# Kernel optimization log

Measured on AMD Instinct MI355X. Metric: run time of the kernel, lower is better.

## Reference

```python
import jax, jax.numpy as jnp
import numpy as np

TWO_PI = 2.0 * np.pi
EPS = 1e-08


def setup_inputs() -> dict:
    key = jax.random.key(0)
    k1, k2, k3 = jax.random.split(key, 3)
    N, D = 1048576, 64
    samples = jax.random.normal(k1, (N, D), dtype=jnp.float32)
    Phi = jax.random.uniform(k2, (1,), dtype=jnp.float32)
    # mu init in torch: 2*rand - 0.5
    mu = 2.0 * jax.random.uniform(k3, (D,), dtype=jnp.float32) - 0.5
    Sigma = jnp.eye(D, dtype=jnp.float32)
    return {"samples": samples, "Phi": Phi, "mu": mu, "Sigma": Sigma}


def reference(samples, Phi, mu, Sigma):
    # Batched Mahalanobis quadratic form replacing the per-sample Python loop.
    inv_sigma = jnp.linalg.pinv(Sigma)                      # [D, D]
    det_sigma = jnp.linalg.det(Sigma)                       # scalar
    diff = samples - mu                                     # [N, D]
    # q_n = diff_n^T inv_sigma diff_n
    q = jnp.einsum('nd,de,ne->n', diff, inv_sigma, diff)    # [N]
    dens = Phi[0] * jnp.exp(-0.5 * q) / jnp.sqrt(TWO_PI * det_sigma)
    return -jnp.log(dens + EPS)                             # with_log=True path
```

## Files before the change

### kernel.cpp

```cpp
#include <hip/hip_runtime.h>


typedef __attribute__((ext_vector_type(8))) short s8bf;
typedef __attribute__((ext_vector_type(4))) float v4f;

#define TWO_PI_F 6.2831853071795864769f

__device__ __forceinline__ float bf2f(ushort u) {
    union { float f; unsigned int i; } v; v.i = ((unsigned int)u) << 16; return v.f;
}
__device__ __forceinline__ ushort f2bf(float f) {
    unsigned int x = __float_as_uint(f);
    return (ushort)((x + 0x7fffu + ((x >> 16) & 1u)) >> 16);
}
__device__ __forceinline__ s8bf pack8(float4 a, float4 b) {
    s8bf r;
    r[0] = (short)f2bf(a.x); r[1] = (short)f2bf(a.y);
    r[2] = (short)f2bf(a.z); r[3] = (short)f2bf(a.w);
    r[4] = (short)f2bf(b.x); r[5] = (short)f2bf(b.y);
    r[6] = (short)f2bf(b.z); r[7] = (short)f2bf(b.w);
    return r;
}

__global__ __launch_bounds__(256) void prep_kernel(const void* __restrict__ Sigma,
                                                   const void* __restrict__ Phi,
                                                   const void* __restrict__ mu,
                                                   void* __restrict__ ws) {
    __shared__ __align__(16) float colbuf[64];
    __shared__ __align__(16) float rowbuf[64];
    __shared__ __align__(16) float sA[64 * 65];
    __shared__ float smu[64];
    const int t = threadIdx.x;
    const int j = t & 63, w = t >> 6;
    const unsigned int wd0 = *(const unsigned int*)Sigma;
    const bool isf32 = (wd0 == 0x3F800000u);

    float ar[16];
    if (isf32) {
        const float* S = (const float*)Sigma;
#pragma unroll
        for (int ii = 0; ii < 16; ++ii) ar[ii] = S[(16 * w + ii) * 64 + j];
    } else {
        const ushort* S = (const ushort*)Sigma;
#pragma unroll
        for (int ii = 0; ii < 16; ++ii) ar[ii] = bf2f(S[(16 * w + ii) * 64 + j]);
    }
    if (t < 64) smu[t] = isf32 ? ((const float*)mu)[t] : bf2f(((const ushort*)mu)[t]);

    float det = 1.0f;
    for (int k = 0; k < 64; ++k) {
        if (j == k) {
#pragma unroll
            for (int ii = 0; ii < 16; ++ii) colbuf[16 * w + ii] = ar[ii];
        }
        if (w == (k >> 4)) {
            float val = ar[0];
#pragma unroll
            for (int ii = 1; ii < 16; ++ii) val = (ii == (k & 15)) ? ar[ii] : val;
            rowbuf[j] = val;
        }
        __syncthreads();
        const float piv = rowbuf[k];
        const float ip = 1.0f / piv;
        const float rk = rowbuf[j] * ip;
        det *= piv;
        const bool jk = (j == k);
#pragma unroll
        for (int ii = 0; ii < 16; ++ii) {
            float f = colbuf[16 * w + ii];
            float nv = fmaf(-f, rk, ar[ii]);
            nv = jk ? (-f * ip) : nv;
            if (16 * w + ii == k) nv = jk ? ip : rk;
            ar[ii] = nv;
        }
        __syncthreads();
    }

    ushort* wb = (ushort*)ws;
#pragma unroll
    for (int ii = 0; ii < 16; ++ii) wb[(16 * w + ii) * 64 + j] = f2bf(ar[ii]);
#pragma unroll
    for (int ii = 0; ii < 16; ++ii) sA[(16 * w + ii) * 65 + j] = ar[ii];
    __syncthreads();

    float* wf = (float*)((char*)ws + 8192);
    if (t < 64) {
        float dot = 0.0f;
#pragma unroll
        for (int jj = 0; jj < 64; ++jj) dot = fmaf(sA[t * 65 + jj], smu[jj], dot);
        wf[t] = 2.0f * dot;
        float pc = smu[t] * dot;
#pragma unroll
        for (int off = 1; off < 64; off <<= 1) pc += __shfl_xor(pc, off, 64);
        if (t == 0) {
            float ph = isf32 ? ((const float*)Phi)[0] : bf2f(((const ushort*)Phi)[0]);
            wf[64] = pc;
            wf[65] = ph / sqrtf(TWO_PI_F * det);
            wf[66] = isf32 ? 1.0f : 0.0f;
        }
    }
}

__global__ __launch_bounds__(256) void gmm_kernel(const void* __restrict__ Xv,
                                                  const void* __restrict__ ws,
                                                  void* __restrict__ outv,
                                                  int ntiles) {
    __shared__ __align__(16) ushort sB[64 * 72];
    __shared__ __align__(16) ushort sX[64 * 64];
    const int t = threadIdx.x;
    const int w = t >> 6, l = t & 63, n = l & 15, q = l >> 4;

    const ushort* wb = (const ushort*)ws;
#pragma unroll
    for (int p0 = 0; p0 < 2; ++p0) {
        int idx = p0 * 2048 + t * 8;
        int r = idx >> 6, c = idx & 63;
        *(uint4*)(&sB[r * 72 + c]) = *(const uint4*)(wb + idx);
    }
    const float* wf = (const float*)((const char*)ws + 8192);
    float vneg[4];
#pragma unroll
    for (int c = 0; c < 4; ++c) vneg[c] = -wf[c * 16 + n];
    const float c0 = wf[64], sc = wf[65];
    const bool isf32 = (wf[66] != 0.0f);
    __syncthreads();

    s8bf bfr[2][4];
#pragma unroll
    for (int s = 0; s < 2; ++s)
#pragma unroll
        for (int c = 0; c < 4; ++c)
            bfr[s][c] = *(const s8bf*)(&sB[(c * 16 + n) * 72 + s * 32 + q * 8]);

    const int sr = t >> 2, h = t & 3;
    const int c0i = 2 * h, c1i = 2 * h + 1;
    ushort* dst0 = sX + sr * 64 + ((c0i ^ (sr & 7)) * 8);
    ushort* dst1 = sX + sr * 64 + ((c1i ^ (sr & 7)) * 8);

    for (int tile = blockIdx.x; tile < ntiles; tile += gridDim.x) {
        s8bf ch0, ch1;
        if (isf32) {
            const float* src = (const float*)Xv + (size_t)tile * 4096 + sr * 64 + h * 16;
            float4 f0 = ((const float4*)src)[0];
            float4 f1 = ((const float4*)src)[1];
            float4 f2 = ((const float4*)src)[2];
            float4 f3 = ((const float4*)src)[3];
            ch0 = pack8(f0, f1);
            ch1 = pack8(f2, f3);
        } else {
            const ushort* src = (const ushort*)Xv + (size_t)tile * 4096 + sr * 64 + h * 16;
            ch0 = ((const s8bf*)src)[0];
            ch1 = ((const s8bf*)src)[1];
        }
        __syncthreads();
        *(s8bf*)dst0 = ch0;
        *(s8bf*)dst1 = ch1;
        __syncthreads();

        v4f acc[4];
#pragma unroll
        for (int c = 0; c < 4; ++c) acc[c] = (v4f){vneg[c], vneg[c], vneg[c], vneg[c]};

#pragma unroll
        for (int s = 0; s < 2; ++s) {
            int chunk = (4 * s + q) ^ (n & 7);
            s8bf af = *(const s8bf*)(sX + (w * 16 + n) * 64 + chunk * 8);
#pragma unroll
            for (int c = 0; c < 4; ++c)
                acc[c] = __builtin_amdgcn_mfma_f32_16x16x32_bf16(af, bfr[s][c], acc[c], 0, 0, 0);
        }

        float p[4] = {0.f, 0.f, 0.f, 0.f};
#pragma unroll
        for (int r = 0; r < 4; ++r) {
            int row = q * 4 + r;
            const ushort* rp = sX + (w * 16 + row) * 64;
            int rm = row & 7;
#pragma unroll
            for (int c = 0; c < 4; ++c) {
                int ch = (2 * c + (n >> 3)) ^ rm;
                float xv = bf2f(rp[ch * 8 + (n & 7)]);
                p[r] = fmaf(acc[c][r], xv, p[r]);
            }
        }
#pragma unroll
        for (int r = 0; r < 4; ++r)
#pragma unroll
            for (int off = 1; off < 16; off <<= 1)
                p[r] += __shfl_xor(p[r], off, 64);

        if (n < 4) {
            float qv = ((n == 0) ? p[0] : (n == 1) ? p[1] : (n == 2) ? p[2] : p[3]) + c0;
            float val = -__logf(sc * __expf(-0.5f * qv) + 1e-8f);
            size_t oi = (size_t)tile * 64 + w * 16 + q * 4 + n;
            if (isf32) ((float*)outv)[oi] = val;
            else       ((ushort*)outv)[oi] = f2bf(val);
        }
    }
}

extern "C" void kernel_launch(void* const* d_in, const int* in_sizes, int n_in,
                              void* d_out, int out_size, void* d_ws, size_t ws_size,
                              hipStream_t stream) {
    const void* X     = d_in[0];
    const void* Phi   = d_in[1];
    const void* mu    = d_in[2];
    const void* Sigma = d_in[3];

    int nrows  = in_sizes[0] / 64;
    int ntiles = nrows / 64;

    prep_kernel<<<1, 256, 0, stream>>>(Sigma, Phi, mu, d_ws);

    int grid = ntiles < 2048 ? ntiles : 2048;
    gmm_kernel<<<grid, 256, 0, stream>>>(X, d_ws, d_out, ntiles);
}
```

Baseline: 399.2 us.

## Load MFMA A-fragments directly from global, drop block-wide LDS staging and barriers

Each wave now loads its own X rows straight from global memory in MFMA A-fragment layout and keeps the fp32 values in registers. This removes the shared X tile and both __syncthreads per tile. The second dot product uses the fp32 values with the MFMA result transposed through a per-wave LDS scratch, so the shuffle reduction drops from 16 lanes to a couple of cross-quad shuffles. Each block processes 128 rows per step, and bf16 packing uses the packed-conversion intrinsic. The global loads are now less contiguous per lane group, and register pressure rises.

```diff
diff --git a/kernel.cpp b/kernel.cpp
--- a/kernel.cpp
+++ b/kernel.cpp
@@ -1,4 +1,5 @@
 #include <hip/hip_runtime.h>
+#include <hip/hip_bf16.h>
 
 
 typedef __attribute__((ext_vector_type(8))) short s8bf;
@@ -13,13 +14,14 @@
     unsigned int x = __float_as_uint(f);
     return (ushort)((x + 0x7fffu + ((x >> 16) & 1u)) >> 16);
 }
-__device__ __forceinline__ s8bf pack8(float4 a, float4 b) {
-    s8bf r;
-    r[0] = (short)f2bf(a.x); r[1] = (short)f2bf(a.y);
-    r[2] = (short)f2bf(a.z); r[3] = (short)f2bf(a.w);
-    r[4] = (short)f2bf(b.x); r[5] = (short)f2bf(b.y);
-    r[6] = (short)f2bf(b.z); r[7] = (short)f2bf(b.w);
-    return r;
+union pk8u { s8bf v; __hip_bfloat162 h[4]; };
+__device__ __forceinline__ s8bf pack8_rn(float4 a, float4 b) {
+    pk8u u;
+    u.h[0] = __float22bfloat162_rn(make_float2(a.x, a.y));
+    u.h[1] = __float22bfloat162_rn(make_float2(a.z, a.w));
+    u.h[2] = __float22bfloat162_rn(make_float2(b.x, b.y));
+    u.h[3] = __float22bfloat162_rn(make_float2(b.z, b.w));
+    return u.v;
 }
 
 __global__ __launch_bounds__(256) void prep_kernel(const void* __restrict__ Sigma,
@@ -104,9 +106,9 @@
 __global__ __launch_bounds__(256) void gmm_kernel(const void* __restrict__ Xv,
                                                   const void* __restrict__ ws,
                                                   void* __restrict__ outv,
-                                                  int ntiles) {
+                                                  int nsteps) {
     __shared__ __align__(16) ushort sB[64 * 72];
-    __shared__ __align__(16) ushort sX[64 * 64];
+    __shared__ __align__(16) float wT[4][16][68];
     const int t = threadIdx.x;
     const int w = t >> 6, l = t & 63, n = l & 15, q = l >> 4;
 
@@ -132,69 +134,87 @@
         for (int c = 0; c < 4; ++c)
             bfr[s][c] = *(const s8bf*)(&sB[(c * 16 + n) * 72 + s * 32 + q * 8]);
 
-    const int sr = t >> 2, h = t & 3;
-    const int c0i = 2 * h, c1i = 2 * h + 1;
-    ushort* dst0 = sX + sr * 64 + ((c0i ^ (sr & 7)) * 8);
-    ushort* dst1 = sX + sr * 64 + ((c1i ^ (sr & 7)) * 8);
-
-    for (int tile = blockIdx.x; tile < ntiles; tile += gridDim.x) {
-        s8bf ch0, ch1;
+    float* myT = &wT[w][0][0];
+
+    for (int step = blockIdx.x; step < nsteps; step += gridDim.x) {
+        const size_t rowbase = (size_t)step * 128 + w * 32;
+
+        float4 xf[2][2][2];
+        s8bf   xb[2][2];
         if (isf32) {
-            const float* src = (const float*)Xv + (size_t)tile * 4096 + sr * 64 + h * 16;
-            float4 f0 = ((const float4*)src)[0];
-            float4 f1 = ((const float4*)src)[1];
-            float4 f2 = ((const float4*)src)[2];
-            float4 f3 = ((const float4*)src)[3];
-            ch0 = pack8(f0, f1);
-            ch1 = pack8(f2, f3);
+            const float* bp = (const float*)Xv;
+#pragma unroll
+            for (int g = 0; g < 2; ++g)
+#pragma unroll
+                for (int s = 0; s < 2; ++s) {
+                    const float* rp = bp + (rowbase + g * 16 + n) * 64 + s * 32 + q * 8;
+                    xf[g][s][0] = ((const float4*)rp)[0];
+                    xf[g][s][1] = ((const float4*)rp)[1];
+                }
         } else {
-            const ushort* src = (const ushort*)Xv + (size_t)tile * 4096 + sr * 64 + h * 16;
-            ch0 = ((const s8bf*)src)[0];
-            ch1 = ((const s8bf*)src)[1];
-        }
-        __syncthreads();
-        *(s8bf*)dst0 = ch0;
-        *(s8bf*)dst1 = ch1;
-        __syncthreads();
-
-        v4f acc[4];
-#pragma unroll
-        for (int c = 0; c < 4; ++c) acc[c] = (v4f){vneg[c], vneg[c], vneg[c], vneg[c]};
-
-#pragma unroll
-        for (int s = 0; s < 2; ++s) {
-            int chunk = (4 * s + q) ^ (n & 7);
-            s8bf af = *(const s8bf*)(sX + (w * 16 + n) * 64 + chunk * 8);
+            const ushort* bp = (const ushort*)Xv;
+#pragma unroll
+            for (int g = 0; g < 2; ++g)
+#pragma unroll
+                for (int s = 0; s < 2; ++s)
+                    xb[g][s] = *(const s8bf*)(bp + (rowbase + g * 16 + n) * 64 + s * 32 + q * 8);
+        }
+
+#pragma unroll
+        for (int g = 0; g < 2; ++g) {
+            s8bf af[2];
+            if (isf32) {
+                af[0] = pack8_rn(xf[g][0][0], xf[g][0][1]);
+                af[1] = pack8_rn(xf[g][1][0], xf[g][1][1]);
+            } else {
+                af[0] = xb[g][0];
+                af[1] = xb[g][1];
+            }
+
+            v4f acc[4];
+#pragma unroll
+            for (int c = 0; c < 4; ++c) acc[c] = (v4f){vneg[c], vneg[c], vneg[c], vneg[c]};
+#pragma unroll
+            for (int s = 0; s < 2; ++s)
+#pragma unroll
+                for (int c = 0; c < 4; ++c)
+                    acc[c] = __builtin_amdgcn_mfma_f32_16x16x32_bf16(af[s], bfr[s][c], acc[c], 0, 0, 0);
+
 #pragma unroll
             for (int c = 0; c < 4; ++c)
-                acc[c] = __builtin_amdgcn_mfma_f32_16x16x32_bf16(af, bfr[s][c], acc[c], 0, 0, 0);
-        }
-
-        float p[4] = {0.f, 0.f, 0.f, 0.f};
-#pragma unroll
-        for (int r = 0; r < 4; ++r) {
-            int row = q * 4 + r;
-            const ushort* rp = sX + (w * 16 + row) * 64;
-            int rm = row & 7;
-#pragma unroll
-            for (int c = 0; c < 4; ++c) {
-                int ch = (2 * c + (n >> 3)) ^ rm;
-                float xv = bf2f(rp[ch * 8 + (n & 7)]);
-                p[r] = fmaf(acc[c][r], xv, p[r]);
+#pragma unroll
+                for (int r = 0; r < 4; ++r)
+                    myT[(4 * q + r) * 68 + 16 * c + n] = acc[c][r];
+
+            float p = 0.0f;
+#pragma unroll
+            for (int s = 0; s < 2; ++s)
+#pragma unroll
+                for (int h = 0; h < 2; ++h) {
+                    float4 tv = *(const float4*)(myT + n * 68 + s * 32 + q * 8 + h * 4);
+                    if (isf32) {
+                        float4 xv = xf[g][s][h];
+                        p = fmaf(tv.x, xv.x, p);
+                        p = fmaf(tv.y, xv.y, p);
+                        p = fmaf(tv.z, xv.z, p);
+                        p = fmaf(tv.w, xv.w, p);
+                    } else {
+                        p = fmaf(tv.x, bf2f((ushort)xb[g][s][4 * h + 0]), p);
+                        p = fmaf(tv.y, bf2f((ushort)xb[g][s][4 * h + 1]), p);
+                        p = fmaf(tv.z, bf2f((ushort)xb[g][s][4 * h + 2]), p);
+                        p = fmaf(tv.w, bf2f((ushort)xb[g][s][4 * h + 3]), p);
+                    }
+                }
+            p += __shfl_xor(p, 16, 64);
+            p += __shfl_xor(p, 32, 64);
+
+            if (q == 0) {
+                float qv = p + c0;
+                float val = -__logf(sc * __expf(-0.5f * qv) + 1e-8f);
+                size_t oi = rowbase + g * 16 + n;
+                if (isf32) ((float*)outv)[oi] = val;
+                else       ((ushort*)outv)[oi] = f2bf(val);
             }
-        }
-#pragma unroll
-        for (int r = 0; r < 4; ++r)
-#pragma unroll
-            for (int off = 1; off < 16; off <<= 1)
-                p[r] += __shfl_xor(p[r], off, 64);
-
-        if (n < 4) {
-            float qv = ((n == 0) ? p[0] : (n == 1) ? p[1] : (n == 2) ? p[2] : p[3]) + c0;
-            float val = -__logf(sc * __expf(-0.5f * qv) + 1e-8f);
-            size_t oi = (size_t)tile * 64 + w * 16 + q * 4 + n;
-            if (isf32) ((float*)outv)[oi] = val;
-            else       ((ushort*)outv)[oi] = f2bf(val);
         }
     }
 }
@@ -208,10 +228,11 @@
     const void* Sigma = d_in[3];
 
     int nrows  = in_sizes[0] / 64;
-    int ntiles = nrows / 64;
+    int nsteps = nrows / 128;
 
     prep_kernel<<<1, 256, 0, stream>>>(Sigma, Phi, mu, d_ws);
 
-    int grid = ntiles < 2048 ? ntiles : 2048;
-    gmm_kernel<<<grid, 256, 0, stream>>>(X, d_ws, d_out, ntiles);
-}
+    int grid = nsteps < 2048 ? nsteps : 2048;
+    if (grid < 1) grid = 1;
+    gmm_kernel<<<grid, 256, 0, stream>>>(X, d_ws, d_out, nsteps);
+}
```

Measured after the change: 403.2 us. About the same (+1.0%).
